# Kernel optimization log

Measured on AMD Instinct MI355X. Metric: run time of the kernel, lower is better.

The kernel has to match this reference:

```python
import jax, jax.numpy as jnp
import numpy as np

B, T, D, N = 2, 2048, 1024, 16
H = D // N  # 64

def setup_inputs() -> dict:
    key = jax.random.key(0)
    ks = jax.random.split(key, 5)
    s = 0.02
    return {
        "x": jax.random.normal(ks[0], (B, T, D), dtype=jnp.float32),
        "w_attn": jax.random.normal(ks[1], (D, 3 * D), dtype=jnp.float32) * s,
        "b_attn": jax.random.normal(ks[2], (3 * D,), dtype=jnp.float32) * s,
        "w_proj": jax.random.normal(ks[3], (D, D), dtype=jnp.float32) * s,
        "b_proj": jax.random.normal(ks[4], (D,), dtype=jnp.float32) * s,
    }

def reference(x, w_attn, b_attn, w_proj, b_proj):
    # qkv projection: (B,T,3D)
    qkv = jnp.einsum('btd,de->bte', x, w_attn) + b_attn
    q, k, v = jnp.split(qkv, 3, axis=-1)
    q = q.reshape(B, T, N, H)
    k = k.reshape(B, T, N, H)
    v = v.reshape(B, T, N, H)
    scale = jnp.asarray(H ** 0.5, dtype=x.dtype)
    # scores: (B, T_q, T_kv, N) -- matches torch einsum 'btnh,bsnh->btsn'
    scores = jnp.einsum('btnh,bsnh->btsn', q, k) / scale
    # causal mask, past_len = 0 (no kv cache)
    causal = jnp.tril(jnp.ones((T, T), dtype=bool))  # (T_q, T_kv)
    scores = jnp.where(causal[None, :, :, None], scores, jnp.asarray(-jnp.inf, dtype=scores.dtype))
    weights = jax.nn.softmax(scores, axis=2)  # softmax over kv axis
    out = jnp.einsum('btsn,bsnh->btnh', weights, v).reshape(B, T, D)
    output = jnp.einsum('btd,de->bte', out, w_proj) + b_proj
    return output, k, v
```

## Files before the change

kernel.cpp:

```cpp
#include <hip/hip_runtime.h>
#include <hip/hip_bf16.h>


typedef __attribute__((ext_vector_type(8))) short bf16x8;
typedef __attribute__((ext_vector_type(4))) float f32x4;

#define MFMA16(a, b, c) __builtin_amdgcn_mfma_f32_16x16x32_bf16(a, b, c, 0, 0, 0)

static constexpr int Bb = 2, Tt = 2048, Dd = 1024, Nn = 16, Hh = 64;
static constexpr float NEG_BIG = -30000.0f;
static constexpr float QSCALE  = 0.125f;

__device__ __forceinline__ short f2bf(float f) {
    __hip_bfloat16 h = __float2bfloat16(f);
    short s; __builtin_memcpy(&s, &h, 2); return s;
}
__device__ __forceinline__ float bf2f(short s) {
    __hip_bfloat16 h; __builtin_memcpy(&h, &s, 2); return __bfloat162float(h);
}
__device__ __forceinline__ bf16x8 cvt8(const float* __restrict__ p) {
    f32x4 a = *(const f32x4*)p, b = *(const f32x4*)(p + 4);
    bf16x8 r;
    #pragma unroll
    for (int j = 0; j < 4; ++j) { r[j] = f2bf(a[j]); r[4 + j] = f2bf(b[j]); }
    return r;
}
__device__ __forceinline__ bf16x8 cvt8s(const float* __restrict__ p, float s) {
    f32x4 a = *(const f32x4*)p, b = *(const f32x4*)(p + 4);
    bf16x8 r;
    #pragma unroll
    for (int j = 0; j < 4; ++j) { r[j] = f2bf(a[j] * s); r[4 + j] = f2bf(b[j] * s); }
    return r;
}

__device__ __forceinline__ void gload16(const short* g, short* l) {
    __builtin_amdgcn_global_load_lds(
        (const __attribute__((address_space(1))) unsigned int*)g,
        (__attribute__((address_space(3))) unsigned int*)l, 16, 0, 0);
}

template<int CTRL>
__device__ __forceinline__ float dppf(float x) {
    int i; __builtin_memcpy(&i, &x, 4);
    i = __builtin_amdgcn_update_dpp(0, i, CTRL, 0xf, 0xf, true);
    float r; __builtin_memcpy(&r, &i, 4); return r;
}
__device__ __forceinline__ float rowmax16(float x) {
    x = fmaxf(x, dppf<0x128>(x)); x = fmaxf(x, dppf<0x124>(x));
    x = fmaxf(x, dppf<0x122>(x)); x = fmaxf(x, dppf<0x121>(x));
    return x;
}
__device__ __forceinline__ float rowsum16(float x) {
    x += dppf<0x128>(x); x += dppf<0x124>(x);
    x += dppf<0x122>(x); x += dppf<0x121>(x);
    return x;
}

__global__ __launch_bounds__(256) void prep(
    const float* __restrict__ x, const float* __restrict__ wa,
    const float* __restrict__ wp,
    short* __restrict__ xb, short* __restrict__ wat, short* __restrict__ wpt)
{
    const int bid = blockIdx.x, tid = threadIdx.x;
    if (bid < 1024) {
        __shared__ float s[64][65];
        const float* src; short* dst; int Nc, k0, n0;
        if (bid < 768) { src = wa; dst = wat; Nc = 3072; k0 = (bid & 15) * 64; n0 = (bid >> 4) * 64; }
        else { int b2 = bid - 768; src = wp; dst = wpt; Nc = 1024; k0 = (b2 & 15) * 64; n0 = (b2 >> 4) * 64; }
        const int row = tid >> 2, cg = (tid & 3) * 16;
        const float* p = src + (size_t)(k0 + row) * Nc + n0 + cg;
        #pragma unroll
        for (int i = 0; i < 4; ++i) {
            f32x4 v = *(const f32x4*)(p + 4 * i);
            #pragma unroll
            for (int j = 0; j < 4; ++j) s[row][cg + 4 * i + j] = v[j];
        }
        __syncthreads();
        bf16x8 o0, o1;
        #pragma unroll
        for (int j = 0; j < 8; ++j) { o0[j] = f2bf(s[cg + j][row]); o1[j] = f2bf(s[cg + 8 + j][row]); }
        short* q = dst + (size_t)(n0 + row) * 1024 + k0 + cg;
        *(bf16x8*)q = o0; *(bf16x8*)(q + 8) = o1;
    } else {
        const size_t base = (size_t)(bid - 1024) * 2048 + tid * 8;
        *(bf16x8*)(xb + base) = cvt8(x + base);
    }
}

template<int MODE>
__global__ __launch_bounds__(MODE == 1 ? 512 : 256, MODE == 1 ? 6 : 4) void gemm128(
    const short* __restrict__ A, const short* __restrict__ Bt,
    const float* __restrict__ bias,
    float* __restrict__ fk, float* __restrict__ fv,
    short* __restrict__ qb, short* __restrict__ kb, short* __restrict__ vt,
    float* __restrict__ fout, int K)
{
    constexpr int BM = (MODE == 1) ? 128 : 64;
    constexpr int BN = (MODE == 1) ? 128 : 64;
    constexpr int MF = (MODE == 1) ? 4 : 2;
    __shared__ short sA[3][BM][32];
    __shared__ short sB[3][BN][32];
    const int tid = threadIdx.x, lane = tid & 63, wave = tid >> 6;
    const int l15 = lane & 15, quad = lane >> 4;

    const int lid = (int)blockIdx.y * (int)gridDim.x + (int)blockIdx.x;
    const int xcd = lid & 7, sidx = lid >> 3;
    int mt, ntl;
    if constexpr (MODE == 1) { mt = (xcd & 3) * 8  + (sidx & 7);  ntl = (xcd >> 2) * 12 + (sidx >> 3); }
    else                     { mt = (xcd & 3) * 16 + (sidx & 15); ntl = (xcd >> 2) * 8  + (sidx >> 4); }
    const int m0 = mt * BM, n0 = ntl * BN;

    const int wr = (MODE == 1) ? (wave >> 2) * 64 : (wave >> 1) * 32;
    const int wc = (MODE == 1) ? (wave & 3) * 32  : (wave & 1) * 32;

    const int rl  = lane >> 2;
    const int csh = (lane & 3) * 8;
    const size_t aOff0 = (size_t)(m0 + wave * 16 + rl) * K + csh;
    const size_t bOff0 = (size_t)(n0 + wave * 16 + rl) * K + csh;

    f32x4 acc[MF][2] = {};

#define STAGE_G(pp, kk)                                                \
    do {                                                               \
        gload16(A  + aOff0 + (kk), &sA[pp][wave * 16][0]);             \
        gload16(Bt + bOff0 + (kk), &sB[pp][wave * 16][0]);             \
    } while (0)

    STAGE_G(0, 0);
    STAGE_G(1, 32);

    int cur = 0;
    for (int k0 = 0; k0 < K; k0 += 32) {
        if (k0 + 32 < K) {
            asm volatile("s_waitcnt vmcnt(2)" ::: "memory");
        } else {
            asm volatile("s_waitcnt vmcnt(0)" ::: "memory");
        }
        __builtin_amdgcn_s_barrier();
        __builtin_amdgcn_sched_barrier(0);

        const int nxt2 = cur >= 1 ? cur - 1 : cur + 2;
        if (k0 + 64 < K) STAGE_G(nxt2, k0 + 64);

        bf16x8 af[MF], bfr[2];
        #pragma unroll
        for (int mt2 = 0; mt2 < MF; ++mt2) af[mt2]  = *(const bf16x8*)&sA[cur][wr + mt2 * 16 + l15][quad * 8];
        #pragma unroll
        for (int nt2 = 0; nt2 < 2; ++nt2)  bfr[nt2] = *(const bf16x8*)&sB[cur][wc + nt2 * 16 + l15][quad * 8];
        #pragma unroll
        for (int mt2 = 0; mt2 < MF; ++mt2)
        #pragma unroll
        for (int nt2 = 0; nt2 < 2; ++nt2)
            acc[mt2][nt2] = MFMA16(af[mt2], bfr[nt2], acc[mt2][nt2]);

        cur = cur < 2 ? cur + 1 : 0;
    }
#undef STAGE_G

    #pragma unroll
    for (int mt2 = 0; mt2 < MF; ++mt2)
    #pragma unroll
    for (int nt2 = 0; nt2 < 2; ++nt2) {
        const int gc = n0 + wc + nt2 * 16 + l15;
        const float bv = bias[gc];
        #pragma unroll
        for (int r = 0; r < 4; ++r) {
            const int grow = m0 + wr + mt2 * 16 + quad * 4 + r;
            const float val = acc[mt2][nt2][r] + bv;
            if (MODE == 1) {
                const int reg = gc >> 10, c = gc & 1023;
                if (reg == 0) {
                    qb[(size_t)grow * 1024 + c] = f2bf(val * QSCALE);
                } else {
                    const int bidx = grow >> 11, tt = grow & 2047;
                    const int nh = c >> 6, h = c & 63;
                    if (reg == 1) {
                        fk[(size_t)grow * 1024 + c] = val;
                        kb[((size_t)(bidx * Nn + nh) * Tt + tt) * Hh + h] = f2bf(val);
                    } else {
                        fv[(size_t)grow * 1024 + c] = val;
                        vt[((size_t)(bidx * Nn + nh) * Hh + h) * Tt + tt] = f2bf(val);
                    }
                }
            } else {
                fout[(size_t)grow * 1024 + gc] = val;
            }
        }
    }
}

__global__ __launch_bounds__(512, 6) void attn5(
    const short* __restrict__ Qb, const short* __restrict__ Kb,
    const short* __restrict__ Vt,
    short* __restrict__ op_part, float* __restrict__ ls_part,
    short* __restrict__ Ob)
{
    const int by = 15 - (int)blockIdx.y;
    const int c  = blockIdx.z;
    if (c && by < 8) return;

    __shared__ short sK[2][64][64];
    __shared__ short sV[2][64][64];
    __shared__ short sP[8][16][72];

    const int tid = threadIdx.x, lane = tid & 63, wave = tid >> 6;
    const int l15 = lane & 15, quad = lane >> 4;
    const int head = blockIdx.x;
    const int b = head >> 4, n = head & 15;
    const int q0w = by * 128 + wave * 16;

    const int gmask = (q0w + 15) >> 6;
    const int g0 = c * 16;
    const int ntmax = min(16, 2 * by + 2 - g0);

    const size_t kvhead = (size_t)head * Tt * Hh;
    const short* kbh = Kb + kvhead;
    const short* vth = Vt + kvhead;

    const short* qp = Qb + ((size_t)b * Tt + q0w + l15) * Dd + n * Hh + quad * 8;
    const bf16x8 qf0 = *(const bf16x8*)qp;
    const bf16x8 qf1 = *(const bf16x8*)(qp + 32);

    const int sr   = wave * 8 + (lane >> 3);
    const int srcb = (((lane & 7) ^ (lane >> 3))) * 8;
    const int swz  = l15 & 7;
    const int bsw  = quad ^ swz;

    f32x4 o_acc[4] = {};
    float lsum[4] = {};

#define STAGE_KV(bb, ktb)                                               \
    do {                                                                \
        gload16(kbh + (size_t)((ktb) + sr) * Hh + srcb, &sK[bb][wave * 8][0]); \
        gload16(vth + (size_t)sr * Tt + (ktb) + srcb,   &sV[bb][wave * 8][0]); \
    } while (0)

    STAGE_KV(0, g0 * 64);
    __syncthreads();

    int buf = 0;
    for (int it = 0; it < ntmax; ++it) {
        const int kt = (g0 + it) * 64;
        if (it + 1 < ntmax) STAGE_KV(buf ^ 1, kt + 64);

        f32x4 s[4] = {};
        #pragma unroll
        for (int jp = 0; jp < 2; ++jp) {
            bf16x8 ka0 = *(const bf16x8*)&sK[buf][32 * jp      + l15][bsw * 8];
            bf16x8 kc0 = *(const bf16x8*)&sK[buf][32 * jp      + l15][(bsw ^ 4) * 8];
            bf16x8 ka1 = *(const bf16x8*)&sK[buf][32 * jp + 16 + l15][bsw * 8];
            bf16x8 kc1 = *(const bf16x8*)&sK[buf][32 * jp + 16 + l15][(bsw ^ 4) * 8];
            __builtin_amdgcn_s_setprio(1);
            s[2 * jp]     = MFMA16(qf0, ka0, s[2 * jp]);
            s[2 * jp]     = MFMA16(qf1, kc0, s[2 * jp]);
            s[2 * jp + 1] = MFMA16(qf0, ka1, s[2 * jp + 1]);
            s[2 * jp + 1] = MFMA16(qf1, kc1, s[2 * jp + 1]);
            __builtin_amdgcn_s_setprio(0);
        }

        const bool masked = (g0 + it >= gmask);
        #pragma unroll
        for (int r = 0; r < 4; ++r) {
            const int row = q0w + quad * 4 + r;
            float x0 = s[0][r], x1 = s[1][r], x2 = s[2][r], x3 = s[3][r];
            if (masked) {
                if (kt + l15      > row) x0 = NEG_BIG;
                if (kt + 16 + l15 > row) x1 = NEG_BIG;
                if (kt + 32 + l15 > row) x2 = NEG_BIG;
                if (kt + 48 + l15 > row) x3 = NEG_BIG;
            }
            const float p0 = __expf(x0), p1 = __expf(x1);
            const float p2 = __expf(x2), p3 = __expf(x3);
            lsum[r] += (p0 + p1) + (p2 + p3);
            short* pw = &sP[wave][quad * 4 + r][l15];
            pw[0] = f2bf(p0); pw[16] = f2bf(p1); pw[32] = f2bf(p2); pw[48] = f2bf(p3);
        }
        __asm__ volatile("s_waitcnt lgkmcnt(0)" ::: "memory");
        bf16x8 pf0 = *(const bf16x8*)&sP[wave][l15][quad * 8];
        bf16x8 pf1 = *(const bf16x8*)&sP[wave][l15][32 + quad * 8];
        #pragma unroll
        for (int hc = 0; hc < 4; ++hc) {
            bf16x8 v0 = *(const bf16x8*)&sV[buf][hc * 16 + l15][bsw * 8];
            bf16x8 v1 = *(const bf16x8*)&sV[buf][hc * 16 + l15][(bsw ^ 4) * 8];
            __builtin_amdgcn_s_setprio(1);
            o_acc[hc] = MFMA16(pf0, v0, o_acc[hc]);
            o_acc[hc] = MFMA16(pf1, v1, o_acc[hc]);
            __builtin_amdgcn_s_setprio(0);
        }
        __syncthreads();
        buf ^= 1;
    }
#undef STAGE_KV

    if (by < 8) {
        short* obw = Ob + ((size_t)b * Tt + q0w) * Dd + n * Hh;
        #pragma unroll
        for (int r = 0; r < 4; ++r) {
            const float rlv = 1.0f / fmaxf(rowsum16(lsum[r]), 1e-20f);
            const int rloc = quad * 4 + r;
            #pragma unroll
            for (int hc = 0; hc < 4; ++hc)
                obw[(size_t)rloc * Dd + hc * 16 + l15] = f2bf(o_acc[hc][r] * rlv);
        }
    } else {
        const int slot = head * 24 + 2 * by - 8 + c;
        short* opw = op_part + ((size_t)slot * 128 + wave * 16) * 64;
        #pragma unroll
        for (int r = 0; r < 4; ++r) {
            const float l = rowsum16(lsum[r]);
            const int rloc = quad * 4 + r;
            if (l15 == 0) ls_part[slot * 128 + wave * 16 + rloc] = l;
            #pragma unroll
            for (int hc = 0; hc < 4; ++hc)
                opw[rloc * 64 + hc * 16 + l15] = f2bf(o_acc[hc][r]);
        }
    }
}

__global__ __launch_bounds__(256) void attn_reduce(
    const short* __restrict__ op_part, const float* __restrict__ ls_part,
    short* __restrict__ Ob)
{
    const int idx = blockIdx.x * 256 + threadIdx.x;
    const int r = idx >> 3;
    const int h0 = (idx & 7) * 8;
    const int head = r >> 10, t = 1024 + (r & 1023);
    const int by = t >> 7, tr = t & 127;
    const int base = head * 24 + 2 * by - 8;

    float acc[8] = {};
    float l = 0.f;
    #pragma unroll
    for (int c = 0; c < 2; ++c) {
        const int slot = base + c;
        bf16x8 v = *(const bf16x8*)(op_part + ((size_t)slot * 128 + tr) * 64 + h0);
        #pragma unroll
        for (int j = 0; j < 8; ++j) acc[j] += bf2f(v[j]);
        l += ls_part[slot * 128 + tr];
    }
    const float rl = 1.0f / fmaxf(l, 1e-20f);
    bf16x8 o;
    #pragma unroll
    for (int j = 0; j < 8; ++j) o[j] = f2bf(acc[j] * rl);
    const int b = head >> 4, n = head & 15;
    *(bf16x8*)(Ob + ((size_t)(b * Tt + t)) * Dd + n * Hh + h0) = o;
}

__global__ __launch_bounds__(256) void gemm_bias_split(
    const float* __restrict__ A, const float* __restrict__ Bm,
    const float* __restrict__ bias,
    float* __restrict__ dst0, float* __restrict__ dst1, float* __restrict__ dst2,
    short* __restrict__ kb, short* __restrict__ vt,
    int K, int Ncols, int Dsplit)
{
    __shared__ short sA[64][40];
    __shared__ short sBt[64][40];
    const int tid  = threadIdx.x;
    const int lane = tid & 63;
    const int wave = tid >> 6;
    const int l15  = lane & 15;
    const int quad = lane >> 4;
    const int m0 = blockIdx.x * 64;
    const int n0 = blockIdx.y * 64;
    const int wm = (wave >> 1) * 32;
    const int wn = (wave & 1) * 32;
    const int ar = tid >> 2, ac = (tid & 3) * 8;
    const int bk = tid >> 3, bc = (tid & 7) * 8;

    f32x4 acc[2][2] = {};
    for (int k0 = 0; k0 < K; k0 += 32) {
        bf16x8 av = cvt8(A  + (size_t)(m0 + ar) * K     + k0 + ac);
        bf16x8 bv = cvt8(Bm + (size_t)(k0 + bk) * Ncols + n0 + bc);
        *(bf16x8*)&sA[ar][ac] = av;
        #pragma unroll
        for (int j = 0; j < 8; ++j) sBt[bc + j][bk] = bv[j];
        __syncthreads();
        bf16x8 a0 = *(const bf16x8*)&sA[wm + l15][quad * 8];
        bf16x8 a1 = *(const bf16x8*)&sA[wm + 16 + l15][quad * 8];
        bf16x8 b0 = *(const bf16x8*)&sBt[wn + l15][quad * 8];
        bf16x8 b1 = *(const bf16x8*)&sBt[wn + 16 + l15][quad * 8];
        acc[0][0] = MFMA16(a0, b0, acc[0][0]);
        acc[0][1] = MFMA16(a0, b1, acc[0][1]);
        acc[1][0] = MFMA16(a1, b0, acc[1][0]);
        acc[1][1] = MFMA16(a1, b1, acc[1][1]);
        __syncthreads();
    }
    #pragma unroll
    for (int i = 0; i < 2; ++i)
    #pragma unroll
    for (int j = 0; j < 2; ++j) {
        const int ncol = n0 + wn + j * 16 + l15;
        const float bvf = bias[ncol];
        float* dbase; int c, which;
        if (ncol < Dsplit)        { dbase = dst0; c = ncol;            which = 0; }
        else if (ncol < 2*Dsplit) { dbase = dst1; c = ncol - Dsplit;   which = 1; }
        else                      { dbase = dst2; c = ncol - 2*Dsplit; which = 2; }
        const int nh = c >> 6, h = c & 63;
        #pragma unroll
        for (int r = 0; r < 4; ++r) {
            const int mrow = m0 + wm + i * 16 + quad * 4 + r;
            const float val = acc[i][j][r] + bvf;
            dbase[(size_t)mrow * Dsplit + c] = val;
            if (which == 1 && kb) {
                const int bidx = mrow >> 11, tt = mrow & 2047;
                kb[((size_t)(bidx * Nn + nh) * Tt + tt) * Hh + h] = f2bf(val);
            } else if (which == 2 && vt) {
                const int bidx = mrow >> 11, tt = mrow & 2047;
                vt[((size_t)(bidx * Nn + nh) * Hh + h) * Tt + tt] = f2bf(val);
            }
        }
    }
}

__global__ __launch_bounds__(256) void attn_fast(
    const float* __restrict__ Q, const short* __restrict__ Kb,
    const short* __restrict__ Vt, float* __restrict__ O)
{
    __shared__ short sP[4][2][16][40];
    const int tid  = threadIdx.x;
    const int lane = tid & 63;
    const int wave = tid >> 6;
    const int l15  = lane & 15;
    const int quad = lane >> 4;
    const int b = blockIdx.x >> 4, n = blockIdx.x & 15;
    const int qg = ((int)gridDim.y - 1 - (int)blockIdx.y) * 4 + wave;
    const int q0 = qg * 16;

    const size_t ohead  = (size_t)b * Tt * Dd + (size_t)n * Hh;
    const size_t kvhead = (size_t)(b * Nn + n) * Tt * Hh;
    const short* kbh = Kb + kvhead;
    const short* vth = Vt + kvhead;

    const float* qrow = Q + ohead + (size_t)(q0 + l15) * Dd;
    const bf16x8 qf0 = cvt8s(qrow + quad * 8, QSCALE);
    const bf16x8 qf1 = cvt8s(qrow + 32 + quad * 8, QSCALE);

    float m_i[4], l_i[4];
    f32x4 o_acc[4] = {};
    #pragma unroll
    for (int r = 0; r < 4; ++r) { m_i[r] = NEG_BIG; l_i[r] = 0.f; }

    int par = 0;
    for (int kt = 0; kt < q0 + 16; kt += 32, par ^= 1) {
        f32x4 s0 = {}, s1 = {};
        {
            const short* k0 = kbh + (size_t)(kt + l15) * Hh + quad * 8;
            bf16x8 k0a = *(const bf16x8*)k0;
            bf16x8 k0b = *(const bf16x8*)(k0 + 32);
            const short* k1 = k0 + 16 * Hh;
            bf16x8 k1a = *(const bf16x8*)k1;
            bf16x8 k1b = *(const bf16x8*)(k1 + 32);
            s0 = MFMA16(qf0, k0a, s0); s0 = MFMA16(qf1, k0b, s0);
            s1 = MFMA16(qf0, k1a, s1); s1 = MFMA16(qf1, k1b, s1);
        }
        const int qr0 = q0 + quad * 4;
        #pragma unroll
        for (int r = 0; r < 4; ++r) {
            float x0 = (kt + l15      > qr0 + r) ? NEG_BIG : s0[r];
            float x1 = (kt + 16 + l15 > qr0 + r) ? NEG_BIG : s1[r];
            const float t  = rowmax16(fmaxf(x0, x1));
            const float mn = fmaxf(m_i[r], t);
            const float alpha = __expf(m_i[r] - mn);
            const float p0 = __expf(x0 - mn);
            const float p1 = __expf(x1 - mn);
            l_i[r] = l_i[r] * alpha + rowsum16(p0 + p1);
            m_i[r] = mn;
            #pragma unroll
            for (int hc = 0; hc < 4; ++hc) o_acc[hc][r] *= alpha;
            sP[wave][par][quad * 4 + r][l15]      = f2bf(p0);
            sP[wave][par][quad * 4 + r][16 + l15] = f2bf(p1);
        }
        __asm__ volatile("s_waitcnt lgkmcnt(0)" ::: "memory");
        bf16x8 pf = *(const bf16x8*)&sP[wave][par][l15][quad * 8];
        #pragma unroll
        for (int hc = 0; hc < 4; ++hc) {
            bf16x8 vf = *(const bf16x8*)(vth + (size_t)(hc * 16 + l15) * Tt + kt + quad * 8);
            o_acc[hc] = MFMA16(pf, vf, o_acc[hc]);
        }
    }
    #pragma unroll
    for (int r = 0; r < 4; ++r) {
        const float rl = 1.0f / fmaxf(l_i[r], 1e-20f);
        #pragma unroll
        for (int hc = 0; hc < 4; ++hc)
            O[ohead + (size_t)(q0 + quad * 4 + r) * Dd + hc * 16 + l15] = o_acc[hc][r] * rl;
    }
}

extern "C" void kernel_launch(void* const* d_in, const int* in_sizes, int n_in,
                              void* d_out, int out_size, void* d_ws, size_t ws_size,
                              hipStream_t stream) {
    const float* x      = (const float*)d_in[0];
    const float* w_attn = (const float*)d_in[1];
    const float* b_attn = (const float*)d_in[2];
    const float* w_proj = (const float*)d_in[3];
    const float* b_proj = (const float*)d_in[4];

    const size_t elems = (size_t)Bb * Tt * Dd;
    float* out  = (float*)d_out;
    float* kout = out  + elems;
    float* vout = kout + elems;

    const size_t NSLOT = (size_t)32 * 24;
    const size_t need_v2 = (4 * elems + (size_t)1024 * 1024 + NSLOT * 128 * 64) * 2
                         + NSLOT * 128 * 4;

    if (ws_size >= need_v2) {
        short* qb  = (short*)d_ws;
        short* kb  = qb + elems;
        short* vt  = kb + elems;
        short* wpt = vt + elems;
        short* xb  = wpt + (size_t)1024 * 1024;
        short* ob  = xb;
        short* op_part = xb + elems;
        float* ls_part = (float*)(op_part + NSLOT * 128 * 64);
        short* wat = op_part;

        prep<<<3072, 256, 0, stream>>>(x, w_attn, w_proj, xb, wat, wpt);
        gemm128<1><<<dim3(32, 24), 512, 0, stream>>>(
            xb, wat, b_attn, kout, vout, qb, kb, vt, nullptr, Dd);
        attn5<<<dim3(Bb * Nn, 16, 2), 512, 0, stream>>>(qb, kb, vt, op_part, ls_part, ob);
        attn_reduce<<<1024, 256, 0, stream>>>(op_part, ls_part, ob);
        gemm128<2><<<dim3(64, 16), 256, 0, stream>>>(
            ob, wpt, b_proj, nullptr, nullptr, nullptr, nullptr, nullptr, out, Dd);
    } else {
        float* o_ws = (float*)d_ws;
        short* kb = (short*)((char*)d_ws + elems * 4);
        short* vt = kb + elems;
        gemm_bias_split<<<dim3((Bb * Tt) / 64, (3 * Dd) / 64), 256, 0, stream>>>(
            x, w_attn, b_attn, out, kout, vout, kb, vt, Dd, 3 * Dd, Dd);
        attn_fast<<<dim3(Bb * Nn, Tt / 64), 256, 0, stream>>>(out, kb, vt, o_ws);
        gemm_bias_split<<<dim3((Bb * Tt) / 64, Dd / 64), 256, 0, stream>>>(
            o_ws, w_proj, b_proj, out, out, out, nullptr, nullptr, Dd, Dd, Dd);
    }
}
```

Measured before the change: 197.2 us.

## Use 256x256 tiles with phased MFMA scheduling for QKV projection GEMM

```diff
diff --git a/kernel.cpp b/kernel.cpp
--- a/kernel.cpp
+++ b/kernel.cpp
@@ -87,38 +87,147 @@
     }
 }
 
-template<int MODE>
-__global__ __launch_bounds__(MODE == 1 ? 512 : 256, MODE == 1 ? 6 : 4) void gemm128(
+__global__ __launch_bounds__(512, 2) void gemm256(
     const short* __restrict__ A, const short* __restrict__ Bt,
     const float* __restrict__ bias,
     float* __restrict__ fk, float* __restrict__ fv,
     short* __restrict__ qb, short* __restrict__ kb, short* __restrict__ vt,
-    float* __restrict__ fout, int K)
+    int K)
 {
-    constexpr int BM = (MODE == 1) ? 128 : 64;
-    constexpr int BN = (MODE == 1) ? 128 : 64;
-    constexpr int MF = (MODE == 1) ? 4 : 2;
-    __shared__ short sA[3][BM][32];
-    __shared__ short sB[3][BN][32];
+    __shared__ short sA[3][256][32];
+    __shared__ short sB[3][256][32];
     const int tid = threadIdx.x, lane = tid & 63, wave = tid >> 6;
     const int l15 = lane & 15, quad = lane >> 4;
+    const int wm = wave >> 2, wn = wave & 3;
 
     const int lid = (int)blockIdx.y * (int)gridDim.x + (int)blockIdx.x;
     const int xcd = lid & 7, sidx = lid >> 3;
-    int mt, ntl;
-    if constexpr (MODE == 1) { mt = (xcd & 3) * 8  + (sidx & 7);  ntl = (xcd >> 2) * 12 + (sidx >> 3); }
-    else                     { mt = (xcd & 3) * 16 + (sidx & 15); ntl = (xcd >> 2) * 8  + (sidx >> 4); }
-    const int m0 = mt * BM, n0 = ntl * BN;
-
-    const int wr = (MODE == 1) ? (wave >> 2) * 64 : (wave >> 1) * 32;
-    const int wc = (MODE == 1) ? (wave & 3) * 32  : (wave & 1) * 32;
+    const int mt  = (xcd & 3) * 4 + (sidx & 3);
+    const int ntl = (xcd >> 2) * 6 + (sidx >> 2);
+    const int m0 = mt * 256, n0 = ntl * 256;
+
+    const int rl = lane >> 2, csh = (lane & 3) * 8;
+
+    f32x4 acc[8][4] = {};
+
+#define STAGE_U(bb, TT, UU)                                                        \
+    do {                                                                           \
+        if constexpr (UU == 0)                                                     \
+            gload16(A  + (size_t)(m0 +       wave * 16 + rl) * K + (TT) * 32 + csh,\
+                    &sA[bb][wave * 16][0]);                                        \
+        else if constexpr (UU == 1)                                                \
+            gload16(A  + (size_t)(m0 + 128 + wave * 16 + rl) * K + (TT) * 32 + csh,\
+                    &sA[bb][128 + wave * 16][0]);                                  \
+        else if constexpr (UU == 2)                                                \
+            gload16(Bt + (size_t)(n0 +       wave * 16 + rl) * K + (TT) * 32 + csh,\
+                    &sB[bb][wave * 16][0]);                                        \
+        else                                                                       \
+            gload16(Bt + (size_t)(n0 + 128 + wave * 16 + rl) * K + (TT) * 32 + csh,\
+                    &sB[bb][128 + wave * 16][0]);                                  \
+    } while (0)
+
+    const int NT = K / 32;
+    STAGE_U(0, 0, 0); STAGE_U(0, 0, 1); STAGE_U(0, 0, 2); STAGE_U(0, 0, 3);
+    STAGE_U(1, 1, 0); STAGE_U(1, 1, 1); STAGE_U(1, 1, 2); STAGE_U(1, 1, 3);
+
+    int cur = 0;
+    for (int T = 0; T < NT; ++T) {
+        if (T + 1 < NT) {
+            asm volatile("s_waitcnt vmcnt(4)" ::: "memory");
+        } else {
+            asm volatile("s_waitcnt vmcnt(0)" ::: "memory");
+        }
+        __builtin_amdgcn_s_barrier();
+        __builtin_amdgcn_sched_barrier(0);
+
+        const int nxt2 = cur >= 1 ? cur - 1 : cur + 2;
+        const bool pf = (T + 2 < NT);
+
+#define PHASE(QM, QN, UU)                                                          \
+    do {                                                                           \
+        if (pf) STAGE_U(nxt2, T + 2, UU);                                          \
+        bf16x8 af0 = *(const bf16x8*)&sA[cur][wm * 128 + QM * 64 +  0 + l15][quad * 8]; \
+        bf16x8 af1 = *(const bf16x8*)&sA[cur][wm * 128 + QM * 64 + 16 + l15][quad * 8]; \
+        bf16x8 af2 = *(const bf16x8*)&sA[cur][wm * 128 + QM * 64 + 32 + l15][quad * 8]; \
+        bf16x8 af3 = *(const bf16x8*)&sA[cur][wm * 128 + QM * 64 + 48 + l15][quad * 8]; \
+        bf16x8 bg0 = *(const bf16x8*)&sB[cur][wn * 64 + QN * 32 +  0 + l15][quad * 8]; \
+        bf16x8 bg1 = *(const bf16x8*)&sB[cur][wn * 64 + QN * 32 + 16 + l15][quad * 8]; \
+        asm volatile("s_waitcnt lgkmcnt(0)" ::: "memory");                         \
+        __builtin_amdgcn_sched_barrier(0);                                         \
+        __builtin_amdgcn_s_setprio(1);                                             \
+        acc[QM * 4 + 0][QN * 2 + 0] = MFMA16(af0, bg0, acc[QM * 4 + 0][QN * 2 + 0]); \
+        acc[QM * 4 + 0][QN * 2 + 1] = MFMA16(af0, bg1, acc[QM * 4 + 0][QN * 2 + 1]); \
+        acc[QM * 4 + 1][QN * 2 + 0] = MFMA16(af1, bg0, acc[QM * 4 + 1][QN * 2 + 0]); \
+        acc[QM * 4 + 1][QN * 2 + 1] = MFMA16(af1, bg1, acc[QM * 4 + 1][QN * 2 + 1]); \
+        acc[QM * 4 + 2][QN * 2 + 0] = MFMA16(af2, bg0, acc[QM * 4 + 2][QN * 2 + 0]); \
+        acc[QM * 4 + 2][QN * 2 + 1] = MFMA16(af2, bg1, acc[QM * 4 + 2][QN * 2 + 1]); \
+        acc[QM * 4 + 3][QN * 2 + 0] = MFMA16(af3, bg0, acc[QM * 4 + 3][QN * 2 + 0]); \
+        acc[QM * 4 + 3][QN * 2 + 1] = MFMA16(af3, bg1, acc[QM * 4 + 3][QN * 2 + 1]); \
+        __builtin_amdgcn_s_setprio(0);                                             \
+        __builtin_amdgcn_s_barrier();                                              \
+    } while (0)
+
+        PHASE(0, 0, 0);
+        PHASE(0, 1, 1);
+        PHASE(1, 0, 2);
+        PHASE(1, 1, 3);
+#undef PHASE
+
+        cur = cur < 2 ? cur + 1 : 0;
+    }
+#undef STAGE_U
+
+    #pragma unroll
+    for (int mt2 = 0; mt2 < 8; ++mt2)
+    #pragma unroll
+    for (int nt2 = 0; nt2 < 4; ++nt2) {
+        const int gc = n0 + wn * 64 + nt2 * 16 + l15;
+        const float bv = bias[gc];
+        #pragma unroll
+        for (int r = 0; r < 4; ++r) {
+            const int grow = m0 + wm * 128 + mt2 * 16 + quad * 4 + r;
+            const float val = acc[mt2][nt2][r] + bv;
+            const int reg = gc >> 10, c = gc & 1023;
+            if (reg == 0) {
+                qb[(size_t)grow * 1024 + c] = f2bf(val * QSCALE);
+            } else {
+                const int bidx = grow >> 11, tt = grow & 2047;
+                const int nh = c >> 6, h = c & 63;
+                if (reg == 1) {
+                    fk[(size_t)grow * 1024 + c] = val;
+                    kb[((size_t)(bidx * Nn + nh) * Tt + tt) * Hh + h] = f2bf(val);
+                } else {
+                    fv[(size_t)grow * 1024 + c] = val;
+                    vt[((size_t)(bidx * Nn + nh) * Hh + h) * Tt + tt] = f2bf(val);
+                }
+            }
+        }
+    }
+}
+
+__global__ __launch_bounds__(256, 4) void gemm64(
+    const short* __restrict__ A, const short* __restrict__ Bt,
+    const float* __restrict__ bias, float* __restrict__ fout, int K)
+{
+    __shared__ short sA[3][64][32];
+    __shared__ short sB[3][64][32];
+    const int tid = threadIdx.x, lane = tid & 63, wave = tid >> 6;
+    const int l15 = lane & 15, quad = lane >> 4;
+
+    const int lid = (int)blockIdx.y * (int)gridDim.x + (int)blockIdx.x;
+    const int xcd = lid & 7, sidx = lid >> 3;
+    const int mt = (xcd & 3) * 16 + (sidx & 15);
+    const int ntl = (xcd >> 2) * 8 + (sidx >> 4);
+    const int m0 = mt * 64, n0 = ntl * 64;
+
+    const int wr = (wave >> 1) * 32, wc = (wave & 1) * 32;
 
     const int rl  = lane >> 2;
     const int csh = (lane & 3) * 8;
     const size_t aOff0 = (size_t)(m0 + wave * 16 + rl) * K + csh;
     const size_t bOff0 = (size_t)(n0 + wave * 16 + rl) * K + csh;
 
-    f32x4 acc[MF][2] = {};
+    f32x4 acc[2][2] = {};
 
 #define STAGE_G(pp, kk)                                                \
     do {                                                               \
@@ -142,13 +251,13 @@
         const int nxt2 = cur >= 1 ? cur - 1 : cur + 2;
         if (k0 + 64 < K) STAGE_G(nxt2, k0 + 64);
 
-        bf16x8 af[MF], bfr[2];
-        #pragma unroll
-        for (int mt2 = 0; mt2 < MF; ++mt2) af[mt2]  = *(const bf16x8*)&sA[cur][wr + mt2 * 16 + l15][quad * 8];
+        bf16x8 af[2], bfr[2];
+        #pragma unroll
+        for (int mt2 = 0; mt2 < 2; ++mt2) af[mt2]  = *(const bf16x8*)&sA[cur][wr + mt2 * 16 + l15][quad * 8];
         #pragma unroll
         for (int nt2 = 0; nt2 < 2; ++nt2)  bfr[nt2] = *(const bf16x8*)&sB[cur][wc + nt2 * 16 + l15][quad * 8];
         #pragma unroll
-        for (int mt2 = 0; mt2 < MF; ++mt2)
+        for (int mt2 = 0; mt2 < 2; ++mt2)
         #pragma unroll
         for (int nt2 = 0; nt2 < 2; ++nt2)
             acc[mt2][nt2] = MFMA16(af[mt2], bfr[nt2], acc[mt2][nt2]);
@@ -158,7 +267,7 @@
 #undef STAGE_G
 
     #pragma unroll
-    for (int mt2 = 0; mt2 < MF; ++mt2)
+    for (int mt2 = 0; mt2 < 2; ++mt2)
     #pragma unroll
     for (int nt2 = 0; nt2 < 2; ++nt2) {
         const int gc = n0 + wc + nt2 * 16 + l15;
@@ -166,25 +275,7 @@
         #pragma unroll
         for (int r = 0; r < 4; ++r) {
             const int grow = m0 + wr + mt2 * 16 + quad * 4 + r;
-            const float val = acc[mt2][nt2][r] + bv;
-            if (MODE == 1) {
-                const int reg = gc >> 10, c = gc & 1023;
-                if (reg == 0) {
-                    qb[(size_t)grow * 1024 + c] = f2bf(val * QSCALE);
-                } else {
-                    const int bidx = grow >> 11, tt = grow & 2047;
-                    const int nh = c >> 6, h = c & 63;
-                    if (reg == 1) {
-                        fk[(size_t)grow * 1024 + c] = val;
-                        kb[((size_t)(bidx * Nn + nh) * Tt + tt) * Hh + h] = f2bf(val);
-                    } else {
-                        fv[(size_t)grow * 1024 + c] = val;
-                        vt[((size_t)(bidx * Nn + nh) * Hh + h) * Tt + tt] = f2bf(val);
-                    }
-                }
-            } else {
-                fout[(size_t)grow * 1024 + gc] = val;
-            }
+            fout[(size_t)grow * 1024 + gc] = acc[mt2][nt2][r] + bv;
         }
     }
 }
@@ -517,12 +608,12 @@
         short* wat = op_part;
 
         prep<<<3072, 256, 0, stream>>>(x, w_attn, w_proj, xb, wat, wpt);
-        gemm128<1><<<dim3(32, 24), 512, 0, stream>>>(
-            xb, wat, b_attn, kout, vout, qb, kb, vt, nullptr, Dd);
+        gemm256<<<dim3(16, 12), 512, 0, stream>>>(
+            xb, wat, b_attn, kout, vout, qb, kb, vt, Dd);
         attn5<<<dim3(Bb * Nn, 16, 2), 512, 0, stream>>>(qb, kb, vt, op_part, ls_part, ob);
         attn_reduce<<<1024, 256, 0, stream>>>(op_part, ls_part, ob);
-        gemm128<2><<<dim3(64, 16), 256, 0, stream>>>(
-            ob, wpt, b_proj, nullptr, nullptr, nullptr, nullptr, nullptr, out, Dd);
+        gemm64<<<dim3(64, 16), 256, 0, stream>>>(
+            ob, wpt, b_proj, out, Dd);
     } else {
         float* o_ws = (float*)d_ws;
         short* kb = (short*)((char*)d_ws + elems * 4);
```

Result: slower. 247.7 us (+25.6%).
